# Performance work log

Hardware: AMD Instinct MI355X
Metric: run time of the kernel (lower is better)

Reference implementation:

```python
import jax, jax.numpy as jnp
import numpy as np

L, D, H = 4096, 1024, 16
HEAD_DIM = D // H
SCALE = 1.0 / float(np.sqrt(HEAD_DIM))


def setup_inputs() -> dict:
    key = jax.random.key(0)
    kq, kk, kv = jax.random.split(key, 3)
    Q = jax.random.normal(kq, (L, D), dtype=jnp.float32)
    K = jax.random.normal(kk, (L, D), dtype=jnp.float32)
    V = jax.random.normal(kv, (L, D), dtype=jnp.float32)
    return {"Q": Q, "K": K, "V": V}


def reference(Q, K, V):
    # [L, D] -> [H, L, head_dim]; contiguous head slices of D (matches the
    # original per-head slicing Q[:, h*hd:(h+1)*hd]).
    q = Q.reshape(L, H, HEAD_DIM).transpose(1, 0, 2)
    k = K.reshape(L, H, HEAD_DIM).transpose(1, 0, 2)
    v = V.reshape(L, H, HEAD_DIM).transpose(1, 0, 2)
    # scores: [H, L, L]
    scores = jnp.einsum('hqd,hkd->hqk', q, k) * SCALE
    probs = jax.nn.softmax(scores, axis=-1)
    out = jnp.einsum('hqk,hkd->hqd', probs, v)  # [H, L, head_dim]
    # merge heads back to [L, D]
    return out.transpose(1, 0, 2).reshape(L, D)
```

## Files before the change

kernel.cpp:

```cpp
#include <hip/hip_runtime.h>
#include <hip/hip_bf16.h>

#define SEQ_L 4096
#define DIM_D 1024
#define NHEAD 16
#define HDIM  64
#define QBLK  64
#define KVB   128
#define NTILE (SEQ_L / KVB)
#define QSCALE 0.180336880f
#define NSHIFT -17.3123405f

typedef __attribute__((ext_vector_type(8))) short bf16x8;
typedef __attribute__((ext_vector_type(4))) short bf16x4;
typedef __attribute__((ext_vector_type(4))) float f32x4;

__device__ __forceinline__ short f2bf(float f) {
    union { float f; unsigned u; } x; x.f = f;
    unsigned r = x.u + 0x7fffu + ((x.u >> 16) & 1u);
    return (short)(r >> 16);
}

__device__ __forceinline__ float fast_exp2(float x) {
#if __has_builtin(__builtin_amdgcn_exp2f)
    return __builtin_amdgcn_exp2f(x);
#else
    return exp2f(x);
#endif
}

__device__ __forceinline__ bf16x4 pk4t(float p0, float p1, float p2, float p3) {
#if __has_builtin(__builtin_amdgcn_perm)
    union { float f; unsigned u; } a0, a1, a2, a3;
    a0.f = p0; a1.f = p1; a2.f = p2; a3.f = p3;
    union { unsigned u[2]; bf16x4 v; } cv;
    cv.u[0] = __builtin_amdgcn_perm(a1.u, a0.u, 0x07060302u);
    cv.u[1] = __builtin_amdgcn_perm(a3.u, a2.u, 0x07060302u);
    return cv.v;
#else
    const bf16x4 r = { f2bf(p0), f2bf(p1), f2bf(p2), f2bf(p3) };
    return r;
#endif
}

__device__ __forceinline__ f32x4 mfma16(bf16x4 a, bf16x4 b, f32x4 c) {
#if __has_builtin(__builtin_amdgcn_mfma_f32_16x16x16bf16_1k)
    return __builtin_amdgcn_mfma_f32_16x16x16bf16_1k(a, b, c, 0, 0, 0);
#else
    asm("v_mfma_f32_16x16x16_bf16 %0, %1, %2, %0" : "+v"(c) : "v"(a), "v"(b));
    return c;
#endif
}

__device__ __forceinline__ void gl16(const void* g, void* l) {
    __builtin_amdgcn_global_load_lds(
        (const __attribute__((address_space(1))) unsigned int*)g,
        (__attribute__((address_space(3))) unsigned int*)l, 16, 0, 0);
}

__global__ void cvt_qk(const float* __restrict__ Q, const float* __restrict__ K,
                       short* __restrict__ Qb, short* __restrict__ Kb) {
    const size_t n8 = (size_t)SEQ_L * DIM_D / 8;
    size_t j = (size_t)blockIdx.x * blockDim.x + threadIdx.x;
    const float* src; short* dst; float sc;
    if (j < n8) { src = Q; dst = Qb; sc = QSCALE; }
    else        { src = K; dst = Kb; sc = 1.0f; j -= n8; }
    const float4 a = *(const float4*)(src + j*8);
    const float4 b = *(const float4*)(src + j*8 + 4);
    bf16x8 v;
    v[0]=f2bf(a.x*sc); v[1]=f2bf(a.y*sc); v[2]=f2bf(a.z*sc); v[3]=f2bf(a.w*sc);
    v[4]=f2bf(b.x*sc); v[5]=f2bf(b.y*sc); v[6]=f2bf(b.z*sc); v[7]=f2bf(b.w*sc);
    *(bf16x8*)(dst + j*8) = v;
}

__global__ void cvt_vT(const float* __restrict__ V, short* __restrict__ VT) {
    __shared__ short tile[64][136];
    const int t = threadIdx.x;
    const int kv0 = blockIdx.x * 128;
    const int h = blockIdx.y;
#pragma unroll
    for (int i = 0; i < 8; ++i) {
        const int idx = i*256 + t;
        const int row = idx >> 4, cg = idx & 15;
        const float4 v = *(const float4*)(V + (size_t)(kv0+row)*DIM_D + h*HDIM + cg*4);
        tile[cg*4+0][row] = f2bf(v.x);
        tile[cg*4+1][row] = f2bf(v.y);
        tile[cg*4+2][row] = f2bf(v.z);
        tile[cg*4+3][row] = f2bf(v.w);
    }
    __syncthreads();
#pragma unroll
    for (int i = 0; i < 4; ++i) {
        const int idx = i*256 + t;
        const int d = idx >> 4, cg = idx & 15;
        *(bf16x8*)(VT + ((size_t)h*HDIM + d)*SEQ_L + kv0 + cg*8) = *(const bf16x8*)&tile[d][cg*8];
    }
}

__launch_bounds__(256, 2)
__global__ void attn_split(const short* __restrict__ Qb, const short* __restrict__ Kb,
                           const short* __restrict__ VT, float* __restrict__ Og) {
    __shared__ union {
        struct { short K[KVB*64]; short V[HDIM*KVB]; } s;
        struct { float Ob0[64*68]; float Ob1[64*68]; float ls[4][64]; } r;
    } u;

    const int t = threadIdx.x;
    const int w = t >> 6, lane = t & 63;
    const int g = lane >> 4, c = lane & 15;
    const int c7 = c & 7;

    const int flat = blockIdx.x;
    const int f2 = (flat & 7) * 128 + (flat >> 3);
    const int h = f2 >> 6, qi = f2 & 63;
    const int qb = qi * QBLK, hc = h * HDIM;

    bf16x8 qa[4][2];
#pragma unroll
    for (int qt = 0; qt < 4; ++qt)
#pragma unroll
        for (int ds = 0; ds < 2; ++ds)
            qa[qt][ds] = *(const bf16x8*)&Qb[(size_t)(qb + qt*16 + c) * DIM_D + hc + ds*32 + g*8];

    f32x4 o[4][4];
    float psum[4];
#pragma unroll
    for (int qt = 0; qt < 4; ++qt) {
        psum[qt] = 0.f;
#pragma unroll
        for (int db = 0; db < 4; ++db) o[qt][db] = (f32x4){0.f,0.f,0.f,0.f};
    }

    int koff[4], vgo[4]; unsigned kdst[4], vdst[4];
#pragma unroll
    for (int i = 0; i < 4; ++i) {
        const int krow = w*32 + i*8 + (lane >> 3);
        koff[i] = krow * DIM_D + (((lane & 7) ^ (krow & 7)) * 8);
        kdst[i] = (unsigned)(w*32 + i*8) * 128;
        const int bb  = 2*i + (lane >> 5);
        const int vkt = bb >> 2, vdb = bb & 3;
        const int lp  = lane & 31;
        vgo[i]  = (vdb*16 + (lp >> 1)) * SEQ_L + w*32 + vkt*16 + (lp & 1)*8;
        vdst[i] = (unsigned)(w*8 + 2*i) * 512;
    }

    const short* Kh  = Kb + hc;
    const short* VTh = VT + (size_t)h * HDIM * SEQ_L;
    const int vslot  = (c*4 + g) * 4;
    const int vwbase = w * 2048;

#pragma unroll
    for (int i = 0; i < 4; ++i) {
        gl16(Kh + koff[i], (char*)u.s.K + kdst[i]);
        gl16(VTh + vgo[i], (char*)u.s.V + vdst[i]);
    }

    for (int tile = 0; tile < NTILE; ++tile) {
        asm volatile("s_waitcnt vmcnt(0)" ::: "memory");
        __builtin_amdgcn_sched_barrier(0);

        bf16x8 kf[2][2];
#pragma unroll
        for (int ktl = 0; ktl < 2; ++ktl)
#pragma unroll
            for (int ds = 0; ds < 2; ++ds)
                kf[ktl][ds] = *(const bf16x8*)&u.s.K[(w*32 + ktl*16 + c)*64 + (((ds*4 + g) ^ c7) * 8)];

        bf16x4 vv[2][4];
#pragma unroll
        for (int ktl = 0; ktl < 2; ++ktl)
#pragma unroll
            for (int db = 0; db < 4; ++db)
                vv[ktl][db] = *(const bf16x4*)&u.s.V[vwbase + (ktl*4 + db)*256 + vslot];

        asm volatile("s_waitcnt lgkmcnt(0)" ::: "memory");
        __builtin_amdgcn_sched_barrier(0);

        if (tile + 1 < NTILE) {
            const short* Kt = Kh + (size_t)(tile + 1) * KVB * DIM_D;
            const short* Vt = VTh + (tile + 1) * KVB;
#pragma unroll
            for (int i = 0; i < 4; ++i) {
                gl16(Kt + koff[i], (char*)u.s.K + kdst[i]);
                gl16(Vt + vgo[i], (char*)u.s.V + vdst[i]);
            }
        }

        __builtin_amdgcn_s_setprio(1);
#pragma unroll
        for (int qt = 0; qt < 4; ++qt) {
            f32x4 a0 = (f32x4){NSHIFT, NSHIFT, NSHIFT, NSHIFT};
            f32x4 a1 = (f32x4){NSHIFT, NSHIFT, NSHIFT, NSHIFT};
            a0 = __builtin_amdgcn_mfma_f32_16x16x32_bf16(kf[0][0], qa[qt][0], a0, 0, 0, 0);
            a0 = __builtin_amdgcn_mfma_f32_16x16x32_bf16(kf[0][1], qa[qt][1], a0, 0, 0, 0);
            a1 = __builtin_amdgcn_mfma_f32_16x16x32_bf16(kf[1][0], qa[qt][0], a1, 0, 0, 0);
            a1 = __builtin_amdgcn_mfma_f32_16x16x32_bf16(kf[1][1], qa[qt][1], a1, 0, 0, 0);

            const float p00 = fast_exp2(a0[0]), p01 = fast_exp2(a0[1]);
            const float p02 = fast_exp2(a0[2]), p03 = fast_exp2(a0[3]);
            const float p10 = fast_exp2(a1[0]), p11 = fast_exp2(a1[1]);
            const float p12 = fast_exp2(a1[2]), p13 = fast_exp2(a1[3]);
            psum[qt] += (p00 + p01) + (p02 + p03) + (p10 + p11) + (p12 + p13);
            const bf16x4 pb0 = pk4t(p00, p01, p02, p03);
            const bf16x4 pb1 = pk4t(p10, p11, p12, p13);

#pragma unroll
            for (int db = 0; db < 4; ++db) {
                o[qt][db] = mfma16(vv[0][db], pb0, o[qt][db]);
                o[qt][db] = mfma16(vv[1][db], pb1, o[qt][db]);
            }
        }
        __builtin_amdgcn_s_setprio(0);
    }

#pragma unroll
    for (int qt = 0; qt < 4; ++qt) {
        psum[qt] += __shfl_xor(psum[qt], 16);
        psum[qt] += __shfl_xor(psum[qt], 32);
    }
    __syncthreads();
    if (lane < 16) {
#pragma unroll
        for (int qt = 0; qt < 4; ++qt) u.r.ls[w][qt*16 + c] = psum[qt];
    }
    if (w == 0) {
#pragma unroll
        for (int qt = 0; qt < 4; ++qt)
#pragma unroll
            for (int db = 0; db < 4; ++db)
                *(f32x4*)&u.r.Ob0[(qt*16 + c)*68 + db*16 + 4*g] = o[qt][db];
    } else if (w == 1) {
#pragma unroll
        for (int qt = 0; qt < 4; ++qt)
#pragma unroll
            for (int db = 0; db < 4; ++db)
                *(f32x4*)&u.r.Ob1[(qt*16 + c)*68 + db*16 + 4*g] = o[qt][db];
    }
    __syncthreads();
    if (w == 2) {
#pragma unroll
        for (int qt = 0; qt < 4; ++qt)
#pragma unroll
            for (int db = 0; db < 4; ++db) {
                f32x4* p = (f32x4*)&u.r.Ob0[(qt*16 + c)*68 + db*16 + 4*g];
                f32x4 s = *p;
#pragma unroll
                for (int r = 0; r < 4; ++r) s[r] += o[qt][db][r];
                *p = s;
            }
    } else if (w == 3) {
#pragma unroll
        for (int qt = 0; qt < 4; ++qt)
#pragma unroll
            for (int db = 0; db < 4; ++db) {
                f32x4* p = (f32x4*)&u.r.Ob1[(qt*16 + c)*68 + db*16 + 4*g];
                f32x4 s = *p;
#pragma unroll
                for (int r = 0; r < 4; ++r) s[r] += o[qt][db][r];
                *p = s;
            }
    }
    __syncthreads();

    {
        const int row = w*16 + (lane >> 2);
        const int cq = lane & 3;
        const float lt = u.r.ls[0][row] + u.r.ls[1][row] + u.r.ls[2][row] + u.r.ls[3][row];
        const float inv = 1.0f / lt;
        float* op = Og + (size_t)(qb + row) * DIM_D + hc + cq*16;
#pragma unroll
        for (int i = 0; i < 4; ++i) {
            float4 v;
            v.x = (u.r.Ob0[row*68 + cq*16 + i*4 + 0] + u.r.Ob1[row*68 + cq*16 + i*4 + 0]) * inv;
            v.y = (u.r.Ob0[row*68 + cq*16 + i*4 + 1] + u.r.Ob1[row*68 + cq*16 + i*4 + 1]) * inv;
            v.z = (u.r.Ob0[row*68 + cq*16 + i*4 + 2] + u.r.Ob1[row*68 + cq*16 + i*4 + 2]) * inv;
            v.w = (u.r.Ob0[row*68 + cq*16 + i*4 + 3] + u.r.Ob1[row*68 + cq*16 + i*4 + 3]) * inv;
            *(float4*)(op + i*4) = v;
        }
    }
}

#define LDKF 72
__global__ void attn_fwd_fallback(const float* __restrict__ Qg, const float* __restrict__ Kg,
                                  const float* __restrict__ Vg, float* __restrict__ Og) {
    __shared__ short Klds[64 * LDKF];
    __shared__ short Vt[HDIM * LDKF];
    __shared__ short Plds[4 * 16 * LDKF];

    const int t = threadIdx.x;
    const int w = t >> 6, lane = t & 63;
    const int g = lane >> 4, c = lane & 15;
    const int qb = blockIdx.x * 64;
    const int h = blockIdx.y, hc = h * HDIM;

    bf16x8 qa[2];
    {
        const int qrow = qb + w * 16 + c;
        const float* qp = Qg + (size_t)qrow * DIM_D + hc + g * 8;
#pragma unroll
        for (int db = 0; db < 2; ++db) {
            bf16x8 a2;
#pragma unroll
            for (int j = 0; j < 8; ++j) a2[j] = f2bf(qp[db * 32 + j] * 0.125f);
            qa[db] = a2;
        }
    }
    float m[4], lsum[4];
    f32x4 o[4];
#pragma unroll
    for (int r = 0; r < 4; ++r) { m[r] = -1e30f; lsum[r] = 0.f; }
#pragma unroll
    for (int db = 0; db < 4; ++db) o[db] = (f32x4){0.f,0.f,0.f,0.f};
    const int tr = t >> 4, tc = t & 15;

    for (int kv0 = 0; kv0 < SEQ_L; kv0 += 64) {
#pragma unroll
        for (int i = 0; i < 4; ++i) {
            const int kv = tr + i * 16;
            const float4 kf4 = *(const float4*)(Kg + (size_t)(kv0 + kv) * DIM_D + hc + tc * 4);
            short4 ks; ks.x = f2bf(kf4.x); ks.y = f2bf(kf4.y); ks.z = f2bf(kf4.z); ks.w = f2bf(kf4.w);
            *(short4*)&Klds[kv * LDKF + tc * 4] = ks;
            const float4 vf4 = *(const float4*)(Vg + (size_t)(kv0 + kv) * DIM_D + hc + tc * 4);
            Vt[(tc*4+0) * LDKF + kv] = f2bf(vf4.x);
            Vt[(tc*4+1) * LDKF + kv] = f2bf(vf4.y);
            Vt[(tc*4+2) * LDKF + kv] = f2bf(vf4.z);
            Vt[(tc*4+3) * LDKF + kv] = f2bf(vf4.w);
        }
        __syncthreads();
        f32x4 acc[4];
#pragma unroll
        for (int kt = 0; kt < 4; ++kt) {
            f32x4 a2 = (f32x4){0.f,0.f,0.f,0.f};
#pragma unroll
            for (int db = 0; db < 2; ++db) {
                bf16x8 kb = *(const bf16x8*)&Klds[(kt*16 + c) * LDKF + db*32 + g*8];
                a2 = __builtin_amdgcn_mfma_f32_16x16x32_bf16(qa[db], kb, a2, 0, 0, 0);
            }
            acc[kt] = a2;
        }
        float tmax[4];
#pragma unroll
        for (int r = 0; r < 4; ++r)
            tmax[r] = fmaxf(fmaxf(acc[0][r], acc[1][r]), fmaxf(acc[2][r], acc[3][r]));
#pragma unroll
        for (int mask = 1; mask < 16; mask <<= 1)
#pragma unroll
            for (int r = 0; r < 4; ++r) tmax[r] = fmaxf(tmax[r], __shfl_xor(tmax[r], mask));
        float alpha[4], ps[4];
#pragma unroll
        for (int r = 0; r < 4; ++r) {
            const float mn = fmaxf(m[r], tmax[r]);
            alpha[r] = __expf(m[r] - mn); m[r] = mn; ps[r] = 0.f;
        }
#pragma unroll
        for (int kt = 0; kt < 4; ++kt)
#pragma unroll
            for (int r = 0; r < 4; ++r) {
                const float p = __expf(acc[kt][r] - m[r]);
                ps[r] += p;
                Plds[(w*16 + g*4 + r) * LDKF + kt*16 + c] = f2bf(p);
            }
#pragma unroll
        for (int mask = 1; mask < 16; mask <<= 1)
#pragma unroll
            for (int r = 0; r < 4; ++r) ps[r] += __shfl_xor(ps[r], mask);
#pragma unroll
        for (int r = 0; r < 4; ++r) lsum[r] = lsum[r] * alpha[r] + ps[r];
#pragma unroll
        for (int db = 0; db < 4; ++db)
#pragma unroll
            for (int r = 0; r < 4; ++r) o[db][r] *= alpha[r];
#pragma unroll
        for (int db = 0; db < 4; ++db)
#pragma unroll
            for (int kb = 0; kb < 2; ++kb) {
                bf16x8 pa = *(const bf16x8*)&Plds[(w*16 + c) * LDKF + kb*32 + g*8];
                bf16x8 vb = *(const bf16x8*)&Vt[(db*16 + c) * LDKF + kb*32 + g*8];
                o[db] = __builtin_amdgcn_mfma_f32_16x16x32_bf16(pa, vb, o[db], 0, 0, 0);
            }
        __syncthreads();
    }
#pragma unroll
    for (int r = 0; r < 4; ++r) {
        const float inv = 1.0f / lsum[r];
        const int qrow = qb + w*16 + g*4 + r;
        float* op = Og + (size_t)qrow * DIM_D + hc;
#pragma unroll
        for (int db = 0; db < 4; ++db) op[db*16 + c] = o[db][r] * inv;
    }
}

extern "C" void kernel_launch(void* const* d_in, const int* in_sizes, int n_in,
                              void* d_out, int out_size, void* d_ws, size_t ws_size,
                              hipStream_t stream) {
    (void)in_sizes; (void)n_in; (void)out_size;
    const float* Q = (const float*)d_in[0];
    const float* K = (const float*)d_in[1];
    const float* V = (const float*)d_in[2];
    float* O = (float*)d_out;

    const size_t n = (size_t)SEQ_L * DIM_D;
    const size_t need = 3 * n * sizeof(short);
    if (ws_size >= need) {
        short* Qb = (short*)d_ws;
        short* Kb = Qb + n;
        short* VT = Qb + 2 * n;
        hipLaunchKernelGGL(cvt_qk, dim3(2 * n / 8 / 256), dim3(256), 0, stream, Q, K, Qb, Kb);
        hipLaunchKernelGGL(cvt_vT, dim3(SEQ_L / 128, NHEAD), dim3(256), 0, stream, V, VT);
        hipLaunchKernelGGL(attn_split, dim3(1024), dim3(256), 0, stream, Qb, Kb, VT, O);
    } else {
        hipLaunchKernelGGL(attn_fwd_fallback, dim3(SEQ_L / 64, NHEAD), dim3(256), 0, stream, Q, K, V, O);
    }
}
```

Measured before the change: 113.2 us.

## Use 16x16x32 MFMA for PV and compute row sums via ones-MFMA

Replaces the pair of 16x16x16 bf16 MFMAs per PV block with a single 16x16x32 MFMA. This requires permuting the K row order in LDS and changing the V^T LDS layout so each lane reads one bf16x8 fragment instead of two bf16x4. The softmax denominator is now an extra MFMA against a vector of ones, replacing the VALU adds and the cross-lane shuffles. The aim is to cut MFMA issue count and VALU work in the inner loop, at the cost of one extra MFMA per query tile and more complex address mapping.

```diff
diff --git a/kernel.cpp b/kernel.cpp
--- a/kernel.cpp
+++ b/kernel.cpp
@@ -40,15 +40,6 @@
 #else
     const bf16x4 r = { f2bf(p0), f2bf(p1), f2bf(p2), f2bf(p3) };
     return r;
-#endif
-}
-
-__device__ __forceinline__ f32x4 mfma16(bf16x4 a, bf16x4 b, f32x4 c) {
-#if __has_builtin(__builtin_amdgcn_mfma_f32_16x16x16bf16_1k)
-    return __builtin_amdgcn_mfma_f32_16x16x16bf16_1k(a, b, c, 0, 0, 0);
-#else
-    asm("v_mfma_f32_16x16x16_bf16 %0, %1, %2, %0" : "+v"(c) : "v"(a), "v"(b));
-    return c;
 #endif
 }
 
@@ -101,7 +92,7 @@
 __global__ void attn_split(const short* __restrict__ Qb, const short* __restrict__ Kb,
                            const short* __restrict__ VT, float* __restrict__ Og) {
     __shared__ union {
-        struct { short K[KVB*64]; short V[HDIM*KVB]; } s;
+        struct { short K[KVB*64]; short V[8192]; } s;
         struct { float Ob0[64*68]; float Ob1[64*68]; float ls[4][64]; } r;
     } u;
 
@@ -122,32 +113,30 @@
         for (int ds = 0; ds < 2; ++ds)
             qa[qt][ds] = *(const bf16x8*)&Qb[(size_t)(qb + qt*16 + c) * DIM_D + hc + ds*32 + g*8];
 
-    f32x4 o[4][4];
-    float psum[4];
+    f32x4 o[4][4], os[4];
 #pragma unroll
     for (int qt = 0; qt < 4; ++qt) {
-        psum[qt] = 0.f;
+        os[qt] = (f32x4){0.f,0.f,0.f,0.f};
 #pragma unroll
         for (int db = 0; db < 4; ++db) o[qt][db] = (f32x4){0.f,0.f,0.f,0.f};
     }
+    const short oneb = (short)0x3F80;
+    const bf16x8 ones8 = { oneb, oneb, oneb, oneb, oneb, oneb, oneb, oneb };
 
     int koff[4], vgo[4]; unsigned kdst[4], vdst[4];
 #pragma unroll
     for (int i = 0; i < 4; ++i) {
-        const int krow = w*32 + i*8 + (lane >> 3);
-        koff[i] = krow * DIM_D + (((lane & 7) ^ (krow & 7)) * 8);
+        const int s = lane >> 3;
+        const int jj = i*8 + s;
+        const int kvp = ((jj & 15) >> 2)*8 + (jj >> 4)*4 + (jj & 3);
+        koff[i] = (w*32 + kvp) * DIM_D + (((lane & 7) ^ s) * 8);
         kdst[i] = (unsigned)(w*32 + i*8) * 128;
-        const int bb  = 2*i + (lane >> 5);
-        const int vkt = bb >> 2, vdb = bb & 3;
-        const int lp  = lane & 31;
-        vgo[i]  = (vdb*16 + (lp >> 1)) * SEQ_L + w*32 + vkt*16 + (lp & 1)*8;
-        vdst[i] = (unsigned)(w*8 + 2*i) * 512;
+        vgo[i]  = (i*16 + c) * SEQ_L + w*32 + g*8;
+        vdst[i] = (unsigned)(w*4096 + i*1024);
     }
 
     const short* Kh  = Kb + hc;
     const short* VTh = VT + (size_t)h * HDIM * SEQ_L;
-    const int vslot  = (c*4 + g) * 4;
-    const int vwbase = w * 2048;
 
 #pragma unroll
     for (int i = 0; i < 4; ++i) {
@@ -166,12 +155,10 @@
             for (int ds = 0; ds < 2; ++ds)
                 kf[ktl][ds] = *(const bf16x8*)&u.s.K[(w*32 + ktl*16 + c)*64 + (((ds*4 + g) ^ c7) * 8)];
 
-        bf16x4 vv[2][4];
-#pragma unroll
-        for (int ktl = 0; ktl < 2; ++ktl)
-#pragma unroll
-            for (int db = 0; db < 4; ++db)
-                vv[ktl][db] = *(const bf16x4*)&u.s.V[vwbase + (ktl*4 + db)*256 + vslot];
+        bf16x8 vv8[4];
+#pragma unroll
+        for (int db = 0; db < 4; ++db)
+            vv8[db] = *(const bf16x8*)&u.s.V[w*2048 + db*512 + (g*16 + c)*8];
 
         asm volatile("s_waitcnt lgkmcnt(0)" ::: "memory");
         __builtin_amdgcn_sched_barrier(0);
@@ -200,28 +187,22 @@
             const float p02 = fast_exp2(a0[2]), p03 = fast_exp2(a0[3]);
             const float p10 = fast_exp2(a1[0]), p11 = fast_exp2(a1[1]);
             const float p12 = fast_exp2(a1[2]), p13 = fast_exp2(a1[3]);
-            psum[qt] += (p00 + p01) + (p02 + p03) + (p10 + p11) + (p12 + p13);
-            const bf16x4 pb0 = pk4t(p00, p01, p02, p03);
-            const bf16x4 pb1 = pk4t(p10, p11, p12, p13);
-
-#pragma unroll
-            for (int db = 0; db < 4; ++db) {
-                o[qt][db] = mfma16(vv[0][db], pb0, o[qt][db]);
-                o[qt][db] = mfma16(vv[1][db], pb1, o[qt][db]);
-            }
+            const bf16x4 pl = pk4t(p00, p01, p02, p03);
+            const bf16x4 ph = pk4t(p10, p11, p12, p13);
+            const bf16x8 pb8 = __builtin_shufflevector(pl, ph, 0, 1, 2, 3, 4, 5, 6, 7);
+
+            os[qt] = __builtin_amdgcn_mfma_f32_16x16x32_bf16(ones8, pb8, os[qt], 0, 0, 0);
+#pragma unroll
+            for (int db = 0; db < 4; ++db)
+                o[qt][db] = __builtin_amdgcn_mfma_f32_16x16x32_bf16(vv8[db], pb8, o[qt][db], 0, 0, 0);
         }
         __builtin_amdgcn_s_setprio(0);
     }
 
-#pragma unroll
-    for (int qt = 0; qt < 4; ++qt) {
-        psum[qt] += __shfl_xor(psum[qt], 16);
-        psum[qt] += __shfl_xor(psum[qt], 32);
-    }
     __syncthreads();
     if (lane < 16) {
 #pragma unroll
-        for (int qt = 0; qt < 4; ++qt) u.r.ls[w][qt*16 + c] = psum[qt];
+        for (int qt = 0; qt < 4; ++qt) u.r.ls[w][qt*16 + c] = os[qt][0];
     }
     if (w == 0) {
 #pragma unroll
```

Result: faster. 106.4 us, median of 2 (-6.0%).
